# Kernel tuning notes

Hardware: AMD Instinct MI355X
Metric: run time of the kernel (lower is better)

The kernel has to match this reference:

```python
import jax, jax.numpy as jnp
import numpy as np

H = 768       # hidden_size
NH = 12       # num_attention_heads
HD = H // NH  # head_size
FF = 3072     # intermediate_size
EPS = 1e-5


def _layernorm(x, g, b):
    m = jnp.mean(x, axis=-1, keepdims=True)
    v = jnp.var(x, axis=-1, keepdims=True)
    return (x - m) * jax.lax.rsqrt(v + EPS) * g + b


def setup_inputs() -> dict:
    key = jax.random.key(0)
    ks = jax.random.split(key, 12)
    B, Sq, Skv = 8, 1024, 1024
    s = 0.02
    return {
        "freq_hidden_states": jax.random.normal(ks[0], (B, Sq, H), jnp.float32),
        "image_hidden_states": jax.random.normal(ks[1], (B, Skv, H), jnp.float32),
        # attention projections (stored [in, out])
        "Wq": jax.random.normal(ks[2], (H, H), jnp.float32) * s,
        "bq": jnp.zeros((H,), jnp.float32),
        "Wk": jax.random.normal(ks[3], (H, H), jnp.float32) * s,
        "bk": jnp.zeros((H,), jnp.float32),
        "Wv": jax.random.normal(ks[4], (H, H), jnp.float32) * s,
        "bv": jnp.zeros((H,), jnp.float32),
        # layernorms
        "ln_att_g": jnp.ones((H,), jnp.float32),
        "ln_att_b": jnp.zeros((H,), jnp.float32),
        "ln_mlp_g": jnp.ones((H,), jnp.float32),
        "ln_mlp_b": jnp.zeros((H,), jnp.float32),
        # MLP
        "W1": jax.random.normal(ks[5], (H, FF), jnp.float32) * s,
        "b1": jnp.zeros((FF,), jnp.float32),
        "W2": jax.random.normal(ks[6], (FF, H), jnp.float32) * s,
        "b2": jnp.zeros((H,), jnp.float32),
    }


def reference(image_hidden_states, freq_hidden_states, Wq, bq, Wk, bk, Wv, bv,
              ln_att_g, ln_att_b, ln_mlp_g, ln_mlp_b, W1, b1, W2, b2):
    B, Sq, _ = freq_hidden_states.shape
    Skv = image_hidden_states.shape[1]
    # cross-attention: query from freq, key/value from image
    q = (freq_hidden_states @ Wq + bq).reshape(B, Sq, NH, HD)
    k = (image_hidden_states @ Wk + bk).reshape(B, Skv, NH, HD)
    v = (image_hidden_states @ Wv + bv).reshape(B, Skv, NH, HD)
    scores = jnp.einsum("bqhd,bkhd->bhqk", q, k) / jnp.sqrt(jnp.float32(HD))
    probs = jax.nn.softmax(scores, axis=-1)
    ctx = jnp.einsum("bhqk,bkhd->bqhd", probs, v).reshape(B, Sq, H)
    # residual with post-LN on the attention output
    h = freq_hidden_states + _layernorm(ctx, ln_att_g, ln_att_b)
    # MLP + residual with post-LN on the MLP output
    mlp = jax.nn.relu(h @ W1 + b1) @ W2 + b2
    return h + _layernorm(mlp, ln_mlp_g, ln_mlp_b)
```

## Files before the change

kernel.cpp:

```cpp
#include <hip/hip_runtime.h>
#include <hip/hip_bf16.h>

#define H 768
#define NH 12
#define HD 64
#define FF 3072
#define SQ 1024
#define SKV 1024

typedef __hip_bfloat16 bf16;
typedef __attribute__((ext_vector_type(8))) short short8;
typedef __attribute__((ext_vector_type(4))) float f32x4;
typedef __attribute__((ext_vector_type(16))) float f32x16;

__device__ inline void gload16(const void* g, void* l) {
  __builtin_amdgcn_global_load_lds((const __attribute__((address_space(1))) void*)g,
                                   (__attribute__((address_space(3))) void*)l, 16, 0, 0);
}

__device__ inline float bf2f(unsigned short u) {
  unsigned int x = ((unsigned int)u) << 16;
  return __builtin_bit_cast(float, x);
}

__device__ inline unsigned int cvtpk(float lo, float hi) {
  unsigned int r;
  asm("v_cvt_pk_bf16_f32 %0, %1, %2" : "=v"(r) : "v"(lo), "v"(hi));
  return r;
}

__device__ inline void cvt_body(const float* __restrict__ src, bf16* __restrict__ dst, int blk) {
  int i = blk * 256 + threadIdx.x;
  float4 v = ((const float4*)src)[i];
  union { unsigned short u[4]; uint2 q; } o;
  bf16 t0 = __float2bfloat16(v.x); o.u[0] = *(unsigned short*)&t0;
  bf16 t1 = __float2bfloat16(v.y); o.u[1] = *(unsigned short*)&t1;
  bf16 t2 = __float2bfloat16(v.z); o.u[2] = *(unsigned short*)&t2;
  bf16 t3 = __float2bfloat16(v.w); o.u[3] = *(unsigned short*)&t3;
  ((uint2*)dst)[i] = o.q;
}

__device__ inline void trans_body(const float* __restrict__ src, bf16* __restrict__ dst,
                                  int Kd, int Nd, int blk, float* tile ) {
  int ntx = Nd >> 5;
  int n0 = (blk % ntx) << 5, k0 = (blk / ntx) << 5;
  int tx = threadIdx.x & 31, ty = threadIdx.x >> 5;
#pragma unroll
  for (int i = 0; i < 4; ++i)
    tile[(ty + i * 8) * 33 + tx] = src[(size_t)(k0 + ty + i * 8) * Nd + n0 + tx];
  __syncthreads();
#pragma unroll
  for (int i = 0; i < 4; ++i)
    dst[(size_t)(n0 + ty + i * 8) * Kd + k0 + tx] = __float2bfloat16(tile[tx * 33 + ty + i * 8]);
}

__global__ __launch_bounds__(256) void prep(
    const float* freq, const float* image, bf16* freqb, bf16* imageb,
    const float* Wq, const float* Wk, const float* Wv, const float* W1, const float* W2,
    bf16* WTq, bf16* WTk, bf16* WTv, bf16* W1T, bf16* W2T, int c1) {
  __shared__ float tile[32 * 33];
  int b = blockIdx.x;
  if (b < c1) { cvt_body(freq, freqb, b); return; }
  b -= c1;
  if (b < c1) { cvt_body(image, imageb, b); return; }
  b -= c1;
  const int TQ = (H / 32) * (H / 32);
  const int T1 = (FF / 32) * (H / 32);
  if (b < TQ)            { trans_body(Wq, WTq, H, H, b, tile); return; }
  b -= TQ;
  if (b < TQ)            { trans_body(Wk, WTk, H, H, b, tile); return; }
  b -= TQ;
  if (b < TQ)            { trans_body(Wv, WTv, H, H, b, tile); return; }
  b -= TQ;
  if (b < T1)            { trans_body(W1, W1T, H, FF, b, tile); return; }
  b -= T1;
  trans_body(W2, W2T, FF, H, b, tile);
}

template <int EPI, int BN>
__global__ __launch_bounds__(256) void gemm_bt(
    const bf16* __restrict__ A, const bf16* __restrict__ BT,
    const float* __restrict__ bias0, const float* __restrict__ bias1,
    void* __restrict__ out0, void* __restrict__ out1, int M, int N, int K) {
  constexpr int SI = BN / 32;
  constexpr int JF = BN / 32;
  __shared__ __align__(16) bf16 lA[128 * 64];
  __shared__ __align__(16) bf16 lB[BN * 64];
  const int t = threadIdx.x;
  const int lane = t & 63, w = t >> 6;
  const int wr = w >> 1, wc = w & 1;
  const int nt = N / BN;
  const int nwg = gridDim.x;
  int bid = blockIdx.x;
  int logical = ((nwg & 7) == 0) ? ((bid & 7) * (nwg >> 3) + (bid >> 3)) : bid;
  const int m0 = (logical / nt) << 7;
  const int n0 = (logical % nt) * BN;

  const f32x4 fz = {0.f, 0.f, 0.f, 0.f};
  f32x4 acc[4][JF];
#pragma unroll
  for (int i = 0; i < 4; ++i)
#pragma unroll
    for (int j = 0; j < JF; ++j) acc[i][j] = fz;

  for (int kt = 0; kt < K; kt += 64) {
#pragma unroll
    for (int i = 0; i < 4; ++i) {
      int idx = i * 256 + t;
      int row = idx >> 3;
      int chunk = (idx & 7) ^ (row & 7);
      gload16(A + (size_t)(m0 + row) * K + kt + chunk * 8, lA + (size_t)(i * 256 + w * 64) * 8);
    }
#pragma unroll
    for (int i = 0; i < SI; ++i) {
      int idx = i * 256 + t;
      int row = idx >> 3;
      int chunk = (idx & 7) ^ (row & 7);
      gload16(BT + (size_t)(n0 + row) * K + kt + chunk * 8, lB + (size_t)(i * 256 + w * 64) * 8);
    }
    __syncthreads();

    short8 af[2][4], bfv[2][JF];
#pragma unroll
    for (int s = 0; s < 2; ++s) {
#pragma unroll
      for (int i = 0; i < 4; ++i) {
        int ra = wr * 64 + i * 16 + (lane & 15);
        int ca = (s * 4 + (lane >> 4)) ^ (ra & 7);
        af[s][i] = *(const short8*)&lA[ra * 64 + ca * 8];
      }
#pragma unroll
      for (int j = 0; j < JF; ++j) {
        int rb = wc * (BN / 2) + j * 16 + (lane & 15);
        int cb = (s * 4 + (lane >> 4)) ^ (rb & 7);
        bfv[s][j] = *(const short8*)&lB[rb * 64 + cb * 8];
      }
    }
#pragma unroll
    for (int s = 0; s < 2; ++s)
#pragma unroll
      for (int i = 0; i < 4; ++i)
#pragma unroll
        for (int j = 0; j < JF; ++j)
          acc[i][j] = __builtin_amdgcn_mfma_f32_16x16x32_bf16(af[s][i], bfv[s][j], acc[i][j], 0, 0, 0);
    __syncthreads();
  }

#pragma unroll
  for (int i = 0; i < 4; ++i) {
    int mbase = m0 + wr * 64 + i * 16 + ((lane >> 4) << 2);
#pragma unroll
    for (int j = 0; j < JF; ++j) {
      int n = n0 + wc * (BN / 2) + j * 16 + (lane & 15);
#pragma unroll
      for (int r = 0; r < 4; ++r) {
        int m = mbase + r;
        float v = acc[i][j][r];
        if (EPI == 0) {
          v = (v + bias0[n]) * 0.180336880f;
          int hlin = (m >> 10) * NH + (n >> 6);
          ((bf16*)out0)[((size_t)hlin * SQ + (m & 1023)) * HD + (n & 63)] = __float2bfloat16(v);
        } else if (EPI == 1) {
          int sel = (n >= H);
          int nn = n - (sel ? H : 0);
          v += (sel ? bias1 : bias0)[nn];
          int hlin = (m >> 10) * NH + (nn >> 6);
          if (!sel)
            ((bf16*)out0)[((size_t)hlin * SKV + (m & 1023)) * HD + (nn & 63)] = __float2bfloat16(v);
          else
            ((bf16*)out1)[((size_t)hlin * HD + (nn & 63)) * SKV + (m & 1023)] = __float2bfloat16(v);
        } else if (EPI == 2) {
          v += bias0[n];
          v = fmaxf(v, 0.f);
          ((bf16*)out0)[(size_t)m * N + n] = __float2bfloat16(v);
        } else {
          v += bias0[n];
          ((bf16*)out0)[(size_t)m * N + n] = __float2bfloat16(v);
        }
      }
    }
  }
}

__global__ __launch_bounds__(256) void attn_fwd(
    const bf16* __restrict__ Q,
    const bf16* __restrict__ Kg_,
    const bf16* __restrict__ VT,
    bf16* __restrict__ ctx, int nblk) {
  __shared__ __align__(16) bf16 Qs[128 * 64];
  __shared__ __align__(16) bf16 Ks[2][64 * 64];
  __shared__ __align__(16) bf16 Vs[2][64 * 64];

  const int t = threadIdx.x, lane = t & 63, w = t >> 6;
  const int hi = lane >> 5, l31 = lane & 31;
  int bid = blockIdx.x;
  int logical = ((nblk & 7) == 0) ? (bid & 7) * (nblk >> 3) + (bid >> 3) : bid;
  const int hl = logical >> 3;
  const int q0 = (logical & 7) << 7;
  const bf16* Qg = Q + ((size_t)hl * SQ + q0) * HD;
  const bf16* Kg = Kg_ + (size_t)hl * SKV * HD;
  const bf16* Vg = VT + (size_t)hl * HD * SKV;

#pragma unroll
  for (int rep = 0; rep < 4; ++rep) {
    int slot = rep * 256 + t;
    int row = slot >> 3, chunk = (slot & 7) ^ (row & 7);
    gload16(Qg + (size_t)row * HD + chunk * 8, (char*)Qs + (size_t)slot * 16);
  }
#pragma unroll
  for (int rep = 0; rep < 2; ++rep) {
    int slot = rep * 256 + t;
    int row = slot >> 3, chunk = (slot & 7) ^ (row & 7);
    gload16(Kg + (size_t)row * HD + chunk * 8, (char*)&Ks[0][0] + (size_t)slot * 16);
    gload16(Vg + (size_t)row * SKV + chunk * 8, (char*)&Vs[0][0] + (size_t)slot * 16);
  }
  __syncthreads();

  short8 aq[4];
#pragma unroll
  for (int ks = 0; ks < 4; ++ks) {
    int row = w * 32 + l31;
    int chunk = (ks * 2 + hi) ^ (row & 7);
    aq[ks] = *(const short8*)&Qs[row * 64 + chunk * 8];
  }

  f32x16 oa0, oa1;
#pragma unroll
  for (int r = 0; r < 16; ++r) { oa0[r] = 0.f; oa1[r] = 0.f; }
  float ls0 = 0.f, ls1 = 0.f;

#pragma unroll 2
  for (int i = 0; i < 16; ++i) {
    const int buf = i & 1;
    if (i < 15) {
      int kvn = (i + 1) << 6;
#pragma unroll
      for (int rep = 0; rep < 2; ++rep) {
        int slot = rep * 256 + t;
        int row = slot >> 3, chunk = (slot & 7) ^ (row & 7);
        gload16(Kg + (size_t)(kvn + row) * HD + chunk * 8, (char*)&Ks[buf ^ 1][0] + (size_t)slot * 16);
        gload16(Vg + (size_t)row * SKV + kvn + chunk * 8, (char*)&Vs[buf ^ 1][0] + (size_t)slot * 16);
      }
    }

    f32x16 sc0, sc1;
#pragma unroll
    for (int r = 0; r < 16; ++r) { sc0[r] = 0.f; sc1[r] = 0.f; }
    __builtin_amdgcn_s_setprio(1);
#pragma unroll
    for (int ks = 0; ks < 4; ++ks) {
      int c0 = ks * 2 + hi;
      int r0 = l31;
      short8 kf0 = *(const short8*)&Ks[buf][r0 * 64 + (c0 ^ (r0 & 7)) * 8];
      sc0 = __builtin_amdgcn_mfma_f32_32x32x16_bf16(kf0, aq[ks], sc0, 0, 0, 0);
      int r1 = 32 + l31;
      short8 kf1 = *(const short8*)&Ks[buf][r1 * 64 + (c0 ^ (r1 & 7)) * 8];
      sc1 = __builtin_amdgcn_mfma_f32_32x32x16_bf16(kf1, aq[ks], sc1, 0, 0, 0);
    }
    __builtin_amdgcn_s_setprio(0);

#pragma unroll
    for (int r = 0; r < 16; ++r) { sc0[r] = exp2f(sc0[r]); ls0 += sc0[r]; }
#pragma unroll
    for (int r = 0; r < 16; ++r) { sc1[r] = exp2f(sc1[r]); ls1 += sc1[r]; }

    short8 pa[4];
#pragma unroll
    for (int k4 = 0; k4 < 4; ++k4) {
      const int base = (k4 & 1) * 8;
      unsigned int p0, p1, qq0, qq1;
      if (k4 & 2) {
        p0 = cvtpk(sc1[base + 0], sc1[base + 1]);
        p1 = cvtpk(sc1[base + 2], sc1[base + 3]);
        qq0 = cvtpk(sc1[base + 4], sc1[base + 5]);
        qq1 = cvtpk(sc1[base + 6], sc1[base + 7]);
      } else {
        p0 = cvtpk(sc0[base + 0], sc0[base + 1]);
        p1 = cvtpk(sc0[base + 2], sc0[base + 3]);
        qq0 = cvtpk(sc0[base + 4], sc0[base + 5]);
        qq1 = cvtpk(sc0[base + 6], sc0[base + 7]);
      }
      asm volatile("v_permlane32_swap_b32 %0, %1" : "+v"(p0), "+v"(qq0));
      asm volatile("v_permlane32_swap_b32 %0, %1" : "+v"(p1), "+v"(qq1));
      union { unsigned int u[4]; short8 s8; } pu;
      pu.u[0] = p0; pu.u[1] = p1; pu.u[2] = qq0; pu.u[3] = qq1;
      pa[k4] = pu.s8;
    }

    __builtin_amdgcn_s_setprio(1);
#pragma unroll
    for (int k4 = 0; k4 < 4; ++k4) {
      int cc = k4 * 2 + hi;
      int r0 = l31;
      short8 vf0 = *(const short8*)&Vs[buf][r0 * 64 + (cc ^ (r0 & 7)) * 8];
      oa0 = __builtin_amdgcn_mfma_f32_32x32x16_bf16(pa[k4], vf0, oa0, 0, 0, 0);
      int r1 = 32 + l31;
      short8 vf1 = *(const short8*)&Vs[buf][r1 * 64 + (cc ^ (r1 & 7)) * 8];
      oa1 = __builtin_amdgcn_mfma_f32_32x32x16_bf16(pa[k4], vf1, oa1, 0, 0, 0);
    }
    __builtin_amdgcn_s_setprio(0);

    __syncthreads();
  }

  float lt = (ls0 + ls1) + __shfl_xor(ls0 + ls1, 32);
  float rlq = 1.0f / lt;
  const int b = hl / NH, hh = hl % NH;
  bf16* outp = ctx + ((size_t)b * SQ + q0 + w * 32) * H + hh * HD;
#pragma unroll
  for (int r = 0; r < 16; ++r) {
    int qo = (r & 3) + 8 * (r >> 2) + 4 * hi;
    float rv = __shfl(rlq, qo);
    bf16* rowp = outp + (size_t)qo * H;
    rowp[l31]      = __float2bfloat16(oa0[r] * rv);
    rowp[32 + l31] = __float2bfloat16(oa1[r] * rv);
  }
}

__global__ __launch_bounds__(256) void ln_res(
    const bf16* __restrict__ x, const float* __restrict__ res,
    const float* __restrict__ g, const float* __restrict__ beta,
    float* __restrict__ o32, bf16* __restrict__ ob, int write_b) {
  const int row = blockIdx.x;
  const int t = threadIdx.x;
  float v[4];
  float s = 0.f, s2 = 0.f;
  if (t < 192) {
    ushort4 xv = ((const ushort4*)(x + (size_t)row * H))[t];
    v[0] = bf2f(xv.x); v[1] = bf2f(xv.y); v[2] = bf2f(xv.z); v[3] = bf2f(xv.w);
#pragma unroll
    for (int k = 0; k < 4; ++k) { s += v[k]; s2 += v[k] * v[k]; }
  } else {
#pragma unroll
    for (int k = 0; k < 4; ++k) v[k] = 0.f;
  }
#pragma unroll
  for (int off = 32; off > 0; off >>= 1) {
    s += __shfl_down(s, off);
    s2 += __shfl_down(s2, off);
  }
  __shared__ float red[8];
  if ((t & 63) == 0) { red[t >> 6] = s; red[4 + (t >> 6)] = s2; }
  __syncthreads();
  float st = red[0] + red[1] + red[2] + red[3];
  float s2t = red[4] + red[5] + red[6] + red[7];
  float mean = st * (1.f / 768.f);
  float var = s2t * (1.f / 768.f) - mean * mean;
  float rs = rsqrtf(var + 1e-5f);
  if (t < 192) {
    float4 rv = ((const float4*)(res + (size_t)row * H))[t];
    float4 gv = ((const float4*)g)[t];
    float4 bv = ((const float4*)beta)[t];
    float4 o;
    o.x = rv.x + (v[0] - mean) * rs * gv.x + bv.x;
    o.y = rv.y + (v[1] - mean) * rs * gv.y + bv.y;
    o.z = rv.z + (v[2] - mean) * rs * gv.z + bv.z;
    o.w = rv.w + (v[3] - mean) * rs * gv.w + bv.w;
    ((float4*)(o32 + (size_t)row * H))[t] = o;
    if (write_b) {
      union { unsigned short u[4]; uint2 q; } ob4;
      bf16 b0 = __float2bfloat16(o.x); ob4.u[0] = *(unsigned short*)&b0;
      bf16 b1 = __float2bfloat16(o.y); ob4.u[1] = *(unsigned short*)&b1;
      bf16 b2 = __float2bfloat16(o.z); ob4.u[2] = *(unsigned short*)&b2;
      bf16 b3 = __float2bfloat16(o.w); ob4.u[3] = *(unsigned short*)&b3;
      ((uint2*)(ob + (size_t)row * H))[t] = ob4.q;
    }
  }
}

extern "C" void kernel_launch(void* const* d_in, const int* in_sizes, int n_in,
                              void* d_out, int out_size, void* d_ws, size_t ws_size,
                              hipStream_t stream) {
  const float* freq  = (const float*)d_in[0];
  const float* image = (const float*)d_in[1];
  const float* Wq = (const float*)d_in[2];
  const float* bq = (const float*)d_in[3];
  const float* Wk = (const float*)d_in[4];
  const float* bk = (const float*)d_in[5];
  const float* Wv = (const float*)d_in[6];
  const float* bv = (const float*)d_in[7];
  const float* g1 = (const float*)d_in[8];
  const float* be1 = (const float*)d_in[9];
  const float* g2 = (const float*)d_in[10];
  const float* be2 = (const float*)d_in[11];
  const float* W1 = (const float*)d_in[12];
  const float* b1 = (const float*)d_in[13];
  const float* W2 = (const float*)d_in[14];
  const float* b2 = (const float*)d_in[15];

  const int Bc = in_sizes[0] / (SQ * H);
  const int M = Bc * SQ;

  char* p = (char*)d_ws;
  bf16* W1T = (bf16*)p;  p += (size_t)FF * H * 2;
  bf16* W2T = (bf16*)p;  p += (size_t)H * FF * 2;
  bf16* ctxb = (bf16*)p; p += (size_t)M * H * 2;
  float* h32 = (float*)p; p += (size_t)M * H * 4;
  bf16* hb = (bf16*)p;   p += (size_t)M * H * 2;
  char* U = p;
  bf16* freqb = (bf16*)U;
  bf16* imageb = (bf16*)(U + (size_t)M * H * 2);
  bf16* WTq   = (bf16*)(U + (size_t)2 * M * H * 2);
  bf16* WTkv  = (bf16*)(U + (size_t)2 * M * H * 2 + (size_t)H * H * 2);
  bf16* Qb    = (bf16*)(U + (size_t)2 * M * H * 2 + (size_t)3 * H * H * 2);
  bf16* Kbuf  = (bf16*)((char*)Qb + (size_t)M * H * 2);
  bf16* VTb   = (bf16*)((char*)Kbuf + (size_t)M * H * 2);
  bf16* mlp1  = (bf16*)U;
  bf16* mlp2b = ctxb;

  int c1 = M * H / 1024;
  int nprep = 2 * c1 + 3 * ((H / 32) * (H / 32)) + (FF / 32) * (H / 32) + (H / 32) * (FF / 32);
  prep<<<nprep, 256, 0, stream>>>(freq, image, freqb, imageb,
                                  Wq, Wk, Wv, W1, W2,
                                  WTq, WTkv, WTkv + (size_t)H * H, W1T, W2T, c1);

  gemm_bt<0, 64><<<(M / 128) * (H / 64), 256, 0, stream>>>(freqb, WTq, bq, nullptr, Qb, nullptr, M, H, H);
  gemm_bt<1, 128><<<(M / 128) * (2 * H / 128), 256, 0, stream>>>(imageb, WTkv, bk, bv, Kbuf, VTb, M, 2 * H, H);
  int nblk = Bc * NH * (SQ / 128);
  attn_fwd<<<nblk, 256, 0, stream>>>(Qb, Kbuf, VTb, ctxb, nblk);
  ln_res<<<M, 256, 0, stream>>>(ctxb, freq, g1, be1, h32, hb, 1);
  gemm_bt<2, 128><<<(M / 128) * (FF / 128), 256, 0, stream>>>(hb, W1T, b1, nullptr, mlp1, nullptr, M, FF, H);
  gemm_bt<3, 64><<<(M / 128) * (H / 64), 256, 0, stream>>>(mlp1, W2T, b2, nullptr, mlp2b, nullptr, M, H, FF);
  ln_res<<<M, 256, 0, stream>>>(mlp2b, h32, g2, be2, (float*)d_out, nullptr, 0);
}
```

Before: 249.6 us.

## Split attention KV range across wave pairs with 512-thread blocks and LDS reduction

```diff
diff --git a/kernel.cpp b/kernel.cpp
--- a/kernel.cpp
+++ b/kernel.cpp
@@ -182,17 +182,18 @@
   }
 }
 
-__global__ __launch_bounds__(256) void attn_fwd(
+__global__ __launch_bounds__(512) void attn_fwd(
     const bf16* __restrict__ Q,
     const bf16* __restrict__ Kg_,
     const bf16* __restrict__ VT,
     bf16* __restrict__ ctx, int nblk) {
-  __shared__ __align__(16) bf16 Qs[128 * 64];
-  __shared__ __align__(16) bf16 Ks[2][64 * 64];
-  __shared__ __align__(16) bf16 Vs[2][64 * 64];
+  __shared__ __align__(16) bf16 Kb[2][2][64 * 64];
+  __shared__ __align__(16) bf16 Vb[2][64 * 64];
+  __shared__ float Lsum[4][32];
 
   const int t = threadIdx.x, lane = t & 63, w = t >> 6;
   const int hi = lane >> 5, l31 = lane & 31;
+  const int qg = w >> 1, par = w & 1;
   int bid = blockIdx.x;
   int logical = ((nblk & 7) == 0) ? (bid & 7) * (nblk >> 3) + (bid >> 3) : bid;
   const int hl = logical >> 3;
@@ -201,28 +202,21 @@
   const bf16* Kg = Kg_ + (size_t)hl * SKV * HD;
   const bf16* Vg = VT + (size_t)hl * HD * SKV;
 
-#pragma unroll
-  for (int rep = 0; rep < 4; ++rep) {
-    int slot = rep * 256 + t;
-    int row = slot >> 3, chunk = (slot & 7) ^ (row & 7);
-    gload16(Qg + (size_t)row * HD + chunk * 8, (char*)Qs + (size_t)slot * 16);
-  }
-#pragma unroll
-  for (int rep = 0; rep < 2; ++rep) {
-    int slot = rep * 256 + t;
-    int row = slot >> 3, chunk = (slot & 7) ^ (row & 7);
-    gload16(Kg + (size_t)row * HD + chunk * 8, (char*)&Ks[0][0] + (size_t)slot * 16);
-    gload16(Vg + (size_t)row * SKV + chunk * 8, (char*)&Vs[0][0] + (size_t)slot * 16);
+  short8 aq[4];
+  {
+    const bf16* qp = Qg + (size_t)(qg * 32 + l31) * HD;
+#pragma unroll
+    for (int ks = 0; ks < 4; ++ks)
+      aq[ks] = *(const short8*)(qp + (ks * 2 + hi) * 8);
+  }
+
+#pragma unroll
+  for (int k = 0; k < 2; ++k) {
+    int row = t >> 3, chunk = (t & 7) ^ (row & 7);
+    gload16(Kg + (size_t)(k * 64 + row) * HD + chunk * 8, (char*)&Kb[0][k][0] + (size_t)t * 16);
+    gload16(Vg + (size_t)row * SKV + k * 64 + chunk * 8, (char*)&Vb[k][0] + (size_t)t * 16);
   }
   __syncthreads();
-
-  short8 aq[4];
-#pragma unroll
-  for (int ks = 0; ks < 4; ++ks) {
-    int row = w * 32 + l31;
-    int chunk = (ks * 2 + hi) ^ (row & 7);
-    aq[ks] = *(const short8*)&Qs[row * 64 + chunk * 8];
-  }
 
   f32x16 oa0, oa1;
 #pragma unroll
@@ -230,19 +224,24 @@
   float ls0 = 0.f, ls1 = 0.f;
 
 #pragma unroll 2
-  for (int i = 0; i < 16; ++i) {
-    const int buf = i & 1;
-    if (i < 15) {
-      int kvn = (i + 1) << 6;
-#pragma unroll
-      for (int rep = 0; rep < 2; ++rep) {
-        int slot = rep * 256 + t;
-        int row = slot >> 3, chunk = (slot & 7) ^ (row & 7);
-        gload16(Kg + (size_t)(kvn + row) * HD + chunk * 8, (char*)&Ks[buf ^ 1][0] + (size_t)slot * 16);
-        gload16(Vg + (size_t)row * SKV + kvn + chunk * 8, (char*)&Vs[buf ^ 1][0] + (size_t)slot * 16);
-      }
-    }
-
+  for (int j = 0; j < 8; ++j) {
+    const int pb = j & 1;
+    if (j > 0) {
+      int kvb = j << 7;
+      int row = t >> 3, chunk = (t & 7) ^ (row & 7);
+#pragma unroll
+      for (int k = 0; k < 2; ++k)
+        gload16(Vg + (size_t)row * SKV + kvb + k * 64 + chunk * 8, (char*)&Vb[k][0] + (size_t)t * 16);
+    }
+    if (j < 7) {
+      int kvb = (j + 1) << 7;
+      int row = t >> 3, chunk = (t & 7) ^ (row & 7);
+#pragma unroll
+      for (int k = 0; k < 2; ++k)
+        gload16(Kg + (size_t)(kvb + k * 64 + row) * HD + chunk * 8, (char*)&Kb[pb ^ 1][k][0] + (size_t)t * 16);
+    }
+
+    const bf16* Kt = &Kb[pb][par][0];
     f32x16 sc0, sc1;
 #pragma unroll
     for (int r = 0; r < 16; ++r) { sc0[r] = 0.f; sc1[r] = 0.f; }
@@ -251,10 +250,10 @@
     for (int ks = 0; ks < 4; ++ks) {
       int c0 = ks * 2 + hi;
       int r0 = l31;
-      short8 kf0 = *(const short8*)&Ks[buf][r0 * 64 + (c0 ^ (r0 & 7)) * 8];
+      short8 kf0 = *(const short8*)&Kt[r0 * 64 + (c0 ^ (r0 & 7)) * 8];
       sc0 = __builtin_amdgcn_mfma_f32_32x32x16_bf16(kf0, aq[ks], sc0, 0, 0, 0);
       int r1 = 32 + l31;
-      short8 kf1 = *(const short8*)&Ks[buf][r1 * 64 + (c0 ^ (r1 & 7)) * 8];
+      short8 kf1 = *(const short8*)&Kt[r1 * 64 + (c0 ^ (r1 & 7)) * 8];
       sc1 = __builtin_amdgcn_mfma_f32_32x32x16_bf16(kf1, aq[ks], sc1, 0, 0, 0);
     }
     __builtin_amdgcn_s_setprio(0);
@@ -287,15 +286,18 @@
       pa[k4] = pu.s8;
     }
 
+    __syncthreads();
+
+    const bf16* Vt = &Vb[par][0];
     __builtin_amdgcn_s_setprio(1);
 #pragma unroll
     for (int k4 = 0; k4 < 4; ++k4) {
       int cc = k4 * 2 + hi;
       int r0 = l31;
-      short8 vf0 = *(const short8*)&Vs[buf][r0 * 64 + (cc ^ (r0 & 7)) * 8];
+      short8 vf0 = *(const short8*)&Vt[r0 * 64 + (cc ^ (r0 & 7)) * 8];
       oa0 = __builtin_amdgcn_mfma_f32_32x32x16_bf16(pa[k4], vf0, oa0, 0, 0, 0);
       int r1 = 32 + l31;
-      short8 vf1 = *(const short8*)&Vs[buf][r1 * 64 + (cc ^ (r1 & 7)) * 8];
+      short8 vf1 = *(const short8*)&Vt[r1 * 64 + (cc ^ (r1 & 7)) * 8];
       oa1 = __builtin_amdgcn_mfma_f32_32x32x16_bf16(pa[k4], vf1, oa1, 0, 0, 0);
     }
     __builtin_amdgcn_s_setprio(0);
@@ -304,16 +306,32 @@
   }
 
   float lt = (ls0 + ls1) + __shfl_xor(ls0 + ls1, 32);
-  float rlq = 1.0f / lt;
-  const int b = hl / NH, hh = hl % NH;
-  bf16* outp = ctx + ((size_t)b * SQ + q0 + w * 32) * H + hh * HD;
-#pragma unroll
-  for (int r = 0; r < 16; ++r) {
-    int qo = (r & 3) + 8 * (r >> 2) + 4 * hi;
-    float rv = __shfl(rlq, qo);
-    bf16* rowp = outp + (size_t)qo * H;
-    rowp[l31]      = __float2bfloat16(oa0[r] * rv);
-    rowp[32 + l31] = __float2bfloat16(oa1[r] * rv);
+  float* C = (float*)&Kb[0][0][0];
+  float* Cg = C + qg * 2048;
+  if (par == 1) {
+#pragma unroll
+    for (int r = 0; r < 16; ++r) {
+      int ro = (r & 3) + 8 * (r >> 2) + 4 * hi;
+      Cg[ro * 64 + l31] = oa0[r];
+      Cg[ro * 64 + 32 + l31] = oa1[r];
+    }
+    if (hi == 0) Lsum[qg][l31] = lt;
+  }
+  __syncthreads();
+  if (par == 0) {
+    float rlq = 1.0f / (lt + Lsum[qg][l31]);
+    const int b = hl / NH, hh = hl % NH;
+    bf16* outp = ctx + ((size_t)b * SQ + q0 + qg * 32) * H + hh * HD;
+#pragma unroll
+    for (int r = 0; r < 16; ++r) {
+      int qo = (r & 3) + 8 * (r >> 2) + 4 * hi;
+      float rv = __shfl(rlq, qo);
+      float v0 = oa0[r] + Cg[qo * 64 + l31];
+      float v1 = oa1[r] + Cg[qo * 64 + 32 + l31];
+      bf16* rowp = outp + (size_t)qo * H;
+      rowp[l31]      = __float2bfloat16(v0 * rv);
+      rowp[32 + l31] = __float2bfloat16(v1 * rv);
+    }
   }
 }
 
@@ -417,7 +435,7 @@
   gemm_bt<0, 64><<<(M / 128) * (H / 64), 256, 0, stream>>>(freqb, WTq, bq, nullptr, Qb, nullptr, M, H, H);
   gemm_bt<1, 128><<<(M / 128) * (2 * H / 128), 256, 0, stream>>>(imageb, WTkv, bk, bv, Kbuf, VTb, M, 2 * H, H);
   int nblk = Bc * NH * (SQ / 128);
-  attn_fwd<<<nblk, 256, 0, stream>>>(Qb, Kbuf, VTb, ctxb, nblk);
+  attn_fwd<<<nblk, 512, 0, stream>>>(Qb, Kbuf, VTb, ctxb, nblk);
   ln_res<<<M, 256, 0, stream>>>(ctxb, freq, g1, be1, h32, hb, 1);
   gemm_bt<2, 128><<<(M / 128) * (FF / 128), 256, 0, stream>>>(hb, W1T, b1, nullptr, mlp1, nullptr, M, FF, H);
   gemm_bt<3, 64><<<(M / 128) * (H / 64), 256, 0, stream>>>(mlp1, W2T, b2, nullptr, mlp2b, nullptr, M, H, FF);
```

After: 250.3 us. Within noise of the previous version (+0.3%).

## Software-pipeline attention: overlap QK^T of next tile with softmax/PV of previous

Applied to the files above, without the earlier changes.

```diff
diff --git a/kernel.cpp b/kernel.cpp
--- a/kernel.cpp
+++ b/kernel.cpp
@@ -187,9 +187,8 @@
     const bf16* __restrict__ Kg_,
     const bf16* __restrict__ VT,
     bf16* __restrict__ ctx, int nblk) {
-  __shared__ __align__(16) bf16 Qs[128 * 64];
-  __shared__ __align__(16) bf16 Ks[2][64 * 64];
-  __shared__ __align__(16) bf16 Vs[2][64 * 64];
+  __shared__ __align__(16) bf16 Kb[2][64 * 64];
+  __shared__ __align__(16) bf16 Vb[3][64 * 64];
 
   const int t = threadIdx.x, lane = t & 63, w = t >> 6;
   const int hi = lane >> 5, l31 = lane & 31;
@@ -201,84 +200,124 @@
   const bf16* Kg = Kg_ + (size_t)hl * SKV * HD;
   const bf16* Vg = VT + (size_t)hl * HD * SKV;
 
-#pragma unroll
-  for (int rep = 0; rep < 4; ++rep) {
-    int slot = rep * 256 + t;
-    int row = slot >> 3, chunk = (slot & 7) ^ (row & 7);
-    gload16(Qg + (size_t)row * HD + chunk * 8, (char*)Qs + (size_t)slot * 16);
-  }
+  short8 aq[4];
+  {
+    const bf16* qp = Qg + (size_t)(w * 32 + l31) * HD;
+#pragma unroll
+    for (int ks = 0; ks < 4; ++ks)
+      aq[ks] = *(const short8*)(qp + (ks * 2 + hi) * 8);
+  }
+
 #pragma unroll
   for (int rep = 0; rep < 2; ++rep) {
     int slot = rep * 256 + t;
     int row = slot >> 3, chunk = (slot & 7) ^ (row & 7);
-    gload16(Kg + (size_t)row * HD + chunk * 8, (char*)&Ks[0][0] + (size_t)slot * 16);
-    gload16(Vg + (size_t)row * SKV + chunk * 8, (char*)&Vs[0][0] + (size_t)slot * 16);
+    gload16(Kg + (size_t)row * HD + chunk * 8, (char*)&Kb[0][0] + (size_t)slot * 16);
+    gload16(Vg + (size_t)row * SKV + chunk * 8, (char*)&Vb[0][0] + (size_t)slot * 16);
   }
   __syncthreads();
 
-  short8 aq[4];
-#pragma unroll
-  for (int ks = 0; ks < 4; ++ks) {
-    int row = w * 32 + l31;
-    int chunk = (ks * 2 + hi) ^ (row & 7);
-    aq[ks] = *(const short8*)&Qs[row * 64 + chunk * 8];
-  }
-
+  f32x16 sc0[2], sc1[2];
   f32x16 oa0, oa1;
 #pragma unroll
   for (int r = 0; r < 16; ++r) { oa0[r] = 0.f; oa1[r] = 0.f; }
   float ls0 = 0.f, ls1 = 0.f;
-
-#pragma unroll 2
-  for (int i = 0; i < 16; ++i) {
-    const int buf = i & 1;
-    if (i < 15) {
-      int kvn = (i + 1) << 6;
+  short8 pa[4];
+
+#pragma unroll
+  for (int j = 0; j < 16; ++j) {
+    const int cur = j & 1, prv = cur ^ 1;
+    if (j < 15) {
+      int kvn = (j + 1) << 6;
 #pragma unroll
       for (int rep = 0; rep < 2; ++rep) {
         int slot = rep * 256 + t;
         int row = slot >> 3, chunk = (slot & 7) ^ (row & 7);
-        gload16(Kg + (size_t)(kvn + row) * HD + chunk * 8, (char*)&Ks[buf ^ 1][0] + (size_t)slot * 16);
-        gload16(Vg + (size_t)row * SKV + kvn + chunk * 8, (char*)&Vs[buf ^ 1][0] + (size_t)slot * 16);
-      }
-    }
-
-    f32x16 sc0, sc1;
-#pragma unroll
-    for (int r = 0; r < 16; ++r) { sc0[r] = 0.f; sc1[r] = 0.f; }
-    __builtin_amdgcn_s_setprio(1);
-#pragma unroll
-    for (int ks = 0; ks < 4; ++ks) {
-      int c0 = ks * 2 + hi;
-      int r0 = l31;
-      short8 kf0 = *(const short8*)&Ks[buf][r0 * 64 + (c0 ^ (r0 & 7)) * 8];
-      sc0 = __builtin_amdgcn_mfma_f32_32x32x16_bf16(kf0, aq[ks], sc0, 0, 0, 0);
-      int r1 = 32 + l31;
-      short8 kf1 = *(const short8*)&Ks[buf][r1 * 64 + (c0 ^ (r1 & 7)) * 8];
-      sc1 = __builtin_amdgcn_mfma_f32_32x32x16_bf16(kf1, aq[ks], sc1, 0, 0, 0);
-    }
-    __builtin_amdgcn_s_setprio(0);
-
-#pragma unroll
-    for (int r = 0; r < 16; ++r) { sc0[r] = exp2f(sc0[r]); ls0 += sc0[r]; }
-#pragma unroll
-    for (int r = 0; r < 16; ++r) { sc1[r] = exp2f(sc1[r]); ls1 += sc1[r]; }
-
-    short8 pa[4];
+        gload16(Kg + (size_t)(kvn + row) * HD + chunk * 8,
+                (char*)&Kb[(j + 1) & 1][0] + (size_t)slot * 16);
+        gload16(Vg + (size_t)row * SKV + kvn + chunk * 8,
+                (char*)&Vb[(j + 1) % 3][0] + (size_t)slot * 16);
+      }
+    }
+
+#pragma unroll
+    for (int r = 0; r < 16; ++r) { sc0[cur][r] = 0.f; sc1[cur][r] = 0.f; }
+    {
+      const bf16* Kt = &Kb[j & 1][0];
+#pragma unroll
+      for (int ks = 0; ks < 4; ++ks) {
+        int c0 = ks * 2 + hi;
+        int r0 = l31;
+        short8 kf0 = *(const short8*)&Kt[r0 * 64 + (c0 ^ (r0 & 7)) * 8];
+        sc0[cur] = __builtin_amdgcn_mfma_f32_32x32x16_bf16(kf0, aq[ks], sc0[cur], 0, 0, 0);
+        int r1 = 32 + l31;
+        short8 kf1 = *(const short8*)&Kt[r1 * 64 + (c0 ^ (r1 & 7)) * 8];
+        sc1[cur] = __builtin_amdgcn_mfma_f32_32x32x16_bf16(kf1, aq[ks], sc1[cur], 0, 0, 0);
+      }
+    }
+
+    if (j > 0) {
+#pragma unroll
+      for (int r = 0; r < 16; ++r) { sc0[prv][r] = exp2f(sc0[prv][r]); ls0 += sc0[prv][r]; }
+#pragma unroll
+      for (int r = 0; r < 16; ++r) { sc1[prv][r] = exp2f(sc1[prv][r]); ls1 += sc1[prv][r]; }
+#pragma unroll
+      for (int k4 = 0; k4 < 4; ++k4) {
+        const int base = (k4 & 1) * 8;
+        unsigned int p0, p1, qq0, qq1;
+        if (k4 & 2) {
+          p0 = cvtpk(sc1[prv][base + 0], sc1[prv][base + 1]);
+          p1 = cvtpk(sc1[prv][base + 2], sc1[prv][base + 3]);
+          qq0 = cvtpk(sc1[prv][base + 4], sc1[prv][base + 5]);
+          qq1 = cvtpk(sc1[prv][base + 6], sc1[prv][base + 7]);
+        } else {
+          p0 = cvtpk(sc0[prv][base + 0], sc0[prv][base + 1]);
+          p1 = cvtpk(sc0[prv][base + 2], sc0[prv][base + 3]);
+          qq0 = cvtpk(sc0[prv][base + 4], sc0[prv][base + 5]);
+          qq1 = cvtpk(sc0[prv][base + 6], sc0[prv][base + 7]);
+        }
+        asm volatile("v_permlane32_swap_b32 %0, %1" : "+v"(p0), "+v"(qq0));
+        asm volatile("v_permlane32_swap_b32 %0, %1" : "+v"(p1), "+v"(qq1));
+        union { unsigned int u[4]; short8 s8; } pu;
+        pu.u[0] = p0; pu.u[1] = p1; pu.u[2] = qq0; pu.u[3] = qq1;
+        pa[k4] = pu.s8;
+      }
+      const bf16* Vt = &Vb[(j - 1) % 3][0];
+#pragma unroll
+      for (int k4 = 0; k4 < 4; ++k4) {
+        int cc = k4 * 2 + hi;
+        int r0 = l31;
+        short8 vf0 = *(const short8*)&Vt[r0 * 64 + (cc ^ (r0 & 7)) * 8];
+        oa0 = __builtin_amdgcn_mfma_f32_32x32x16_bf16(pa[k4], vf0, oa0, 0, 0, 0);
+        int r1 = 32 + l31;
+        short8 vf1 = *(const short8*)&Vt[r1 * 64 + (cc ^ (r1 & 7)) * 8];
+        oa1 = __builtin_amdgcn_mfma_f32_32x32x16_bf16(pa[k4], vf1, oa1, 0, 0, 0);
+      }
+    }
+
+    __syncthreads();
+  }
+
+  {
+    const int prv = 15 & 1;
+#pragma unroll
+    for (int r = 0; r < 16; ++r) { sc0[prv][r] = exp2f(sc0[prv][r]); ls0 += sc0[prv][r]; }
+#pragma unroll
+    for (int r = 0; r < 16; ++r) { sc1[prv][r] = exp2f(sc1[prv][r]); ls1 += sc1[prv][r]; }
 #pragma unroll
     for (int k4 = 0; k4 < 4; ++k4) {
       const int base = (k4 & 1) * 8;
       unsigned int p0, p1, qq0, qq1;
       if (k4 & 2) {
-        p0 = cvtpk(sc1[base + 0], sc1[base + 1]);
-        p1 = cvtpk(sc1[base + 2], sc1[base + 3]);
-        qq0 = cvtpk(sc1[base + 4], sc1[base + 5]);
-        qq1 = cvtpk(sc1[base + 6], sc1[base + 7]);
+        p0 = cvtpk(sc1[prv][base + 0], sc1[prv][base + 1]);
+        p1 = cvtpk(sc1[prv][base + 2], sc1[prv][base + 3]);
+        qq0 = cvtpk(sc1[prv][base + 4], sc1[prv][base + 5]);
+        qq1 = cvtpk(sc1[prv][base + 6], sc1[prv][base + 7]);
       } else {
-        p0 = cvtpk(sc0[base + 0], sc0[base + 1]);
-        p1 = cvtpk(sc0[base + 2], sc0[base + 3]);
-        qq0 = cvtpk(sc0[base + 4], sc0[base + 5]);
-        qq1 = cvtpk(sc0[base + 6], sc0[base + 7]);
+        p0 = cvtpk(sc0[prv][base + 0], sc0[prv][base + 1]);
+        p1 = cvtpk(sc0[prv][base + 2], sc0[prv][base + 3]);
+        qq0 = cvtpk(sc0[prv][base + 4], sc0[prv][base + 5]);
+        qq1 = cvtpk(sc0[prv][base + 6], sc0[prv][base + 7]);
       }
       asm volatile("v_permlane32_swap_b32 %0, %1" : "+v"(p0), "+v"(qq0));
       asm volatile("v_permlane32_swap_b32 %0, %1" : "+v"(p1), "+v"(qq1));
@@ -286,21 +325,17 @@
       pu.u[0] = p0; pu.u[1] = p1; pu.u[2] = qq0; pu.u[3] = qq1;
       pa[k4] = pu.s8;
     }
-
-    __builtin_amdgcn_s_setprio(1);
+    const bf16* Vt = &Vb[0][0];
 #pragma unroll
     for (int k4 = 0; k4 < 4; ++k4) {
       int cc = k4 * 2 + hi;
       int r0 = l31;
-      short8 vf0 = *(const short8*)&Vs[buf][r0 * 64 + (cc ^ (r0 & 7)) * 8];
+      short8 vf0 = *(const short8*)&Vt[r0 * 64 + (cc ^ (r0 & 7)) * 8];
       oa0 = __builtin_amdgcn_mfma_f32_32x32x16_bf16(pa[k4], vf0, oa0, 0, 0, 0);
       int r1 = 32 + l31;
-      short8 vf1 = *(const short8*)&Vs[buf][r1 * 64 + (cc ^ (r1 & 7)) * 8];
+      short8 vf1 = *(const short8*)&Vt[r1 * 64 + (cc ^ (r1 & 7)) * 8];
       oa1 = __builtin_amdgcn_mfma_f32_32x32x16_bf16(pa[k4], vf1, oa1, 0, 0, 0);
     }
-    __builtin_amdgcn_s_setprio(0);
-
-    __syncthreads();
   }
 
   float lt = (ls0 + ls1) + __shfl_xor(ls0 + ls1, 32);
```

Result: slower. 382.9 us (+53.4%).
